# Optimization experiments

Hardware: AMD Instinct MI355X
Metric: run time of the kernel (lower is better)

The kernel has to match this reference:

```python
import jax, jax.numpy as jnp
from jax import lax
import numpy as np

B, C, O, NF, H, W = 4, 64, 64, 64, 128, 128
DK = 3
K = DK * DK
PAD = DK // 2


def setup_inputs() -> dict:
    key = jax.random.key(0)
    k0, k1, k2, k3 = jax.random.split(key, 4)
    inputs = jax.random.normal(k0, (B, C, H, W), jnp.float32)
    feat = jax.random.normal(k1, (B, NF, H, W), jnp.float32)
    # small offset-conv weights keep learned offsets in a realistic sub-pixel range
    om_w = jax.random.normal(k2, (C * 3 * K, NF, 3, 3), jnp.float32) * 0.02
    om_b = jnp.zeros((C * 3 * K,), jnp.float32)
    dc_w = jax.random.normal(k3, (O, C, DK, DK), jnp.float32) * (1.0 / np.sqrt(C * K))
    dc_b = jnp.zeros((O,), jnp.float32)
    return dict(inputs=inputs, feat=feat, om_w=om_w, om_b=om_b, dc_w=dc_w, dc_b=dc_b)


def _gather(img, y, x):
    # img: [B,C,H,W]; y,x: int32 [B,C,K,H,W]; zero outside bounds
    valid = (y >= 0) & (y < H) & (x >= 0) & (x < W)
    yc = jnp.clip(y, 0, H - 1)
    xc = jnp.clip(x, 0, W - 1)
    idx = (yc * W + xc).reshape(B, C, K, H * W)
    flat = img.reshape(B, C, 1, H * W)
    v = jnp.take_along_axis(flat, idx, axis=3).reshape(B, C, K, H, W)
    return jnp.where(valid, v, 0.0)


def _forward(inputs, feat, om_w, om_b, dc_w, dc_b):
    # offset/mask conv: nf -> in_nc*3*K, 3x3, pad 1
    off_msk = lax.conv_general_dilated(
        feat, om_w, (1, 1), ((1, 1), (1, 1)),
        dimension_numbers=('NCHW', 'OIHW', 'NCHW')) + om_b[None, :, None, None]
    # offsets interleaved (y,x) per kernel tap per deformable group (= channel)
    off = off_msk[:, :C * 2 * K].reshape(B, C, K, 2, H, W)
    msk = jax.nn.sigmoid(off_msk[:, C * 2 * K:]).reshape(B, C, K, H, W)

    ky = (jnp.arange(K) // DK - PAD).astype(jnp.float32)  # [K]
    kx = (jnp.arange(K) % DK - PAD).astype(jnp.float32)
    hg = jnp.arange(H, dtype=jnp.float32)
    wg = jnp.arange(W, dtype=jnp.float32)
    py = hg[None, None, None, :, None] + ky[None, None, :, None, None] + off[:, :, :, 0]  # [B,C,K,H,W]
    px = wg[None, None, None, None, :] + kx[None, None, :, None, None] + off[:, :, :, 1]

    y0f = jnp.floor(py); x0f = jnp.floor(px)
    wy = py - y0f; wx = px - x0f
    y0 = y0f.astype(jnp.int32); x0 = x0f.astype(jnp.int32)
    y1 = y0 + 1; x1 = x0 + 1

    v00 = _gather(inputs, y0, x0)
    v01 = _gather(inputs, y0, x1)
    v10 = _gather(inputs, y1, x0)
    v11 = _gather(inputs, y1, x1)
    sampled = ((1 - wy) * (1 - wx) * v00 + (1 - wy) * wx * v01
               + wy * (1 - wx) * v10 + wy * wx * v11) * msk  # [B,C,K,H,W]

    out = jnp.einsum('bckhw,ock->bohw', sampled, dc_w.reshape(O, C, K))
    out = out + dc_b[None, :, None, None]
    return jax.nn.relu(out)


def reference(inputs, feat, om_w, om_b, dc_w, dc_b):
    return _forward(inputs, feat, om_w, om_b, dc_w, dc_b)
```

## Files before the change

### kernel.cpp

```cpp
#include <hip/hip_runtime.h>
#include <hip/hip_bf16.h>

typedef __bf16 bf16;
typedef __bf16 bf16x8 __attribute__((ext_vector_type(8)));
typedef __bf16 bf16x4 __attribute__((ext_vector_type(4)));
typedef float f32x4 __attribute__((ext_vector_type(4)));
typedef float f32x2 __attribute__((ext_vector_type(2)));
typedef float f32x2u __attribute__((ext_vector_type(2))) __attribute__((aligned(4)));
typedef int  i32x4 __attribute__((ext_vector_type(4)));

#define MFMA16(a, b, c) __builtin_amdgcn_mfma_f32_16x16x32_bf16((a), (b), (c), 0, 0, 0)

static constexpr size_t FEATS_OFF = 0;
static constexpr size_t OMW3_OFF  = 8388608;
static constexpr size_t DCW_OFF   = OMW3_OFF + 1990656;
static constexpr size_t SC_OFF    = DCW_OFF + 73728;
static constexpr size_t PAD_OFF   = SC_OFF + 9216;


__global__ void prep_featS(const float* __restrict__ feat, bf16* __restrict__ featS) {
    const int hh = blockIdx.x, b = blockIdx.y;
    __shared__ float t[64][129];
    for (int i = threadIdx.x; i < 64 * 32; i += 256) {
        int cf = i >> 5, q = i & 31;
        const float* src = feat + ((size_t)(b * 64 + cf) * 128 + hh) * 128 + q * 4;
        t[cf][q * 4 + 0] = src[0];
        t[cf][q * 4 + 1] = src[1];
        t[cf][q * 4 + 2] = src[2];
        t[cf][q * 4 + 3] = src[3];
    }
    __syncthreads();
    for (int i = threadIdx.x; i < 1024; i += 256) {
        int px = i >> 3, cfb = i & 7;
        int sb = cfb ^ (px & 7);
        bf16x8 v;
#pragma unroll
        for (int e = 0; e < 8; ++e) v[e] = (bf16)t[cfb * 8 + e][px];
        *(bf16x8*)(featS + ((size_t)((b * 128 + hh) * 128 + px) << 6) + sb * 8) = v;
    }
}

__global__ void prep_weights(const float* __restrict__ om_w, const float* __restrict__ om_b,
                             const float* __restrict__ dc_w,
                             bf16* __restrict__ omw3, bf16* __restrict__ dcw2p,
                             float* __restrict__ scf) {
    int i = blockIdx.x * 256 + threadIdx.x;
    if (i < 995328) {
        int e = i & 511, lane = e >> 3, j = e & 7;
        int q = i >> 9;
        int t = q % 3, q2 = q / 3, kk = q2 % 18, ct = q2 / 18;
        int ck = ct * 16 + (lane & 15);
        int kcol = kk * 32 + (lane >> 4) * 8 + j;
        int tap = kcol >> 6, cf = kcol & 63;
        int ch = (t < 2) ? (ck * 2 + t) : (1152 + ck);
        omw3[i] = (bf16)om_w[ch * 576 + cf * 9 + tap];
    }
    if (i < 36864) {
        int j = i & 7, lane = (i >> 3) & 63, ot = (i >> 9) & 3, win = i >> 11;
        int o = ot * 16 + (lane & 15);
        int ck = win * 32 + (lane >> 4) * 8 + j;
        dcw2p[i] = (bf16)dc_w[o * 576 + ck];
    }
    if (i < 576) {
        int ck = i;
        int c = ck / 9, kd = ck - 9 * c, kq = kd / 3, kx = kd - 3 * kq;
        int pr = ck >> 1, lo = ck & 1;
        scf[pr * 8 + 0 + lo] = om_b[ck * 2]     + (float)(kq + 2);
        scf[pr * 8 + 2 + lo] = om_b[ck * 2 + 1] + (float)(kx + 2);
        scf[pr * 8 + 4 + lo] = om_b[1152 + ck];
        scf[pr * 8 + 6 + lo] = __uint_as_float((unsigned)(c * 17956));
    }
}

__global__ void prep_pad(const float* __restrict__ inputs, float* __restrict__ pad) {
    int yy = blockIdx.x, bc = blockIdx.y, xx = threadIdx.x;
    if (xx >= 134) return;
    float v = 0.f;
    if (yy >= 3 && yy <= 130 && xx >= 3 && xx <= 130)
        v = inputs[(size_t)bc * 16384 + (yy - 3) * 128 + (xx - 3)];
    pad[((size_t)bc * 134 + yy) * 134 + xx] = v;
}


__global__ void __launch_bounds__(256, 4)
deform_fused(const float* __restrict__ pad,
             const bf16* __restrict__ featS,
             const bf16* __restrict__ omw3,
             const bf16* __restrict__ dcw2p,
             const f32x4* __restrict__ sconst,
             const float* __restrict__ dcb,
             float* __restrict__ out)
{
    const int bid = blockIdx.x;
    const int P0 = (bid & 1) << 6;
    const int h = (bid >> 1) & 127;
    const int b = bid >> 8;
    const int tid = threadIdx.x;
    const int lane = tid & 63;
    const int wid_s = __builtin_amdgcn_readfirstlane(tid >> 6);
    const int l15 = lane & 15, g = lane >> 4;

    __shared__ __align__(16) unsigned char smem[25344 + 8192];
    char* featB = (char*)smem;
    char* sampB = (char*)smem + 25344;

    for (int i = tid; i < 6336; i += 256) ((unsigned*)featB)[i] = 0u;
    __syncthreads();
    {
        const int s0 = (P0 == 0) ? 0 : 63;
        const int q0 = (P0 == 0) ? 1 : 0;
        for (int i = tid; i < 1560; i += 256) {
            int ky = i / 520, rem = i - ky * 520, row = rem >> 3, c = rem & 7;
            int hh = h - 1 + ky;
            if ((unsigned)hh < 128u) {
                const char* src = (const char*)featS
                    + (((size_t)(b * 128 + hh) * 128 + s0 + row) << 7) + c * 16;
                *(i32x4*)(featB + ((ky * 66 + q0 + row) << 7) + c * 16) = *(const i32x4*)src;
            }
        }
    }
    __syncthreads();

    int fb[18];
#pragma unroll
    for (int kk = 0; kk < 18; ++kk) {
        const int tap = kk >> 1;
        const int kyp = tap / 3, kxp = tap - 3 * kyp;
        const int q = l15 + kxp;
        fb[kk] = (kyp * 66 + q) * 128 + ((((kk & 1) * 4 + g) ^ ((q + 7) & 7)) << 4);
    }

    f32x4 acc2[4];
#pragma unroll
    for (int u = 0; u < 4; ++u) acc2[u] = (f32x4){0.f, 0.f, 0.f, 0.f};

    const bf16* omw3_l = omw3 + lane * 8;
    const bf16* dcw_l  = dcw2p + lane * 8;
    const float* padb0 = pad + (size_t)b * 64 * 17956;
    const f32x2 hb2 = {(float)h, (float)h};
    const f32x2 fx2 = {(float)(P0 + l15), (float)(P0 + l15)};
    const int g4 = g * 4;

#pragma unroll 1
    for (int blk = 0; blk < 9; ++blk) {
        f32x4 acc1[3][4];
#pragma unroll
        for (int t = 0; t < 3; ++t)
#pragma unroll
            for (int nf = 0; nf < 4; ++nf) acc1[t][nf] = (f32x4){0.f, 0.f, 0.f, 0.f};

        const int abase = (blk * 4 + wid_s) * 27648;

#pragma unroll
        for (int kk = 0; kk < 18; ++kk) {
            bf16x8 a0 = *(const bf16x8*)(omw3_l + abase + ((kk * 3 + 0) << 9));
            bf16x8 a1 = *(const bf16x8*)(omw3_l + abase + ((kk * 3 + 1) << 9));
            bf16x8 a2 = *(const bf16x8*)(omw3_l + abase + ((kk * 3 + 2) << 9));
            bf16x8 bfr[4];
#pragma unroll
            for (int nf = 0; nf < 4; ++nf)
                bfr[nf] = *(const bf16x8*)(featB + fb[kk] + nf * 2048);
            __builtin_amdgcn_s_setprio(1);
#pragma unroll
            for (int nf = 0; nf < 4; ++nf) {
                acc1[0][nf] = MFMA16(a0, bfr[nf], acc1[0][nf]);
                acc1[1][nf] = MFMA16(a1, bfr[nf], acc1[1][nf]);
                acc1[2][nf] = MFMA16(a2, bfr[nf], acc1[2][nf]);
            }
            __builtin_amdgcn_s_setprio(0);
        }

        bf16x8 aK0 = *(const bf16x8*)(dcw_l + ((blk * 8 + wid_s) << 9));
        bf16x8 aK1 = *(const bf16x8*)(dcw_l + ((blk * 8 + 4 + wid_s) << 9));

        const f32x4* scB = sconst + (blk * 64 + wid_s * 16);
        f32x4 e0A = scB[g4 + 0], e1A = scB[g4 + 1];
        f32x4 e0B = scB[g4 + 2], e1B = scB[g4 + 3];
        f32x2 yb[2], xb[2], mb[2];
        unsigned co[2][2];
        yb[0] = f32x2{e0A.x, e0A.y} + hb2;
        xb[0] = f32x2{e0A.z, e0A.w} + fx2;
        mb[0] = f32x2{e1A.x, e1A.y};
        co[0][0] = __float_as_uint(e1A.z); co[0][1] = __float_as_uint(e1A.w);
        yb[1] = f32x2{e0B.x, e0B.y} + hb2;
        xb[1] = f32x2{e0B.z, e0B.w} + fx2;
        mb[1] = f32x2{e1B.x, e1B.y};
        co[1][0] = __float_as_uint(e1B.z); co[1][1] = __float_as_uint(e1B.w);

#pragma unroll
        for (int nf = 0; nf < 4; ++nf) {
            float s[4];
#pragma unroll
            for (int pi = 0; pi < 2; ++pi) {
                f32x2 py = f32x2{acc1[0][nf][2 * pi], acc1[0][nf][2 * pi + 1]} + yb[pi];
                f32x2 px = f32x2{acc1[1][nf][2 * pi], acc1[1][nf][2 * pi + 1]} + xb[pi];
                f32x2 lg = f32x2{acc1[2][nf][2 * pi], acc1[2][nf][2 * pi + 1]} + mb[pi];
#pragma unroll
                for (int e = 0; e < 2; ++e) {
                    float pyc = __builtin_amdgcn_fmed3f(py[e], 0.5f, 132.5f);
                    float pxc = __builtin_amdgcn_fmed3f(px[e], 0.5f, 132.5f);
                    int y0 = (int)pyc, x0 = (int)pxc;
                    float wy = __builtin_amdgcn_fractf(pyc);
                    float wx = __builtin_amdgcn_fractf(pxc);
                    unsigned off = co[pi][e] + (unsigned)(y0 * 134 + x0);
                    f32x2u t0 = *(const f32x2u*)(padb0 + off);
                    f32x2u t1 = *(const f32x2u*)(padb0 + off + 134);
                    float top = t0.x + wx * (t0.y - t0.x);
                    float bot = t1.x + wx * (t1.y - t1.x);
                    float bil = top + wy * (bot - top);
                    float mk = __builtin_amdgcn_rcpf(1.f + __expf(-lg[e]));
                    s[2 * pi + e] = bil * mk;
                }
            }
            bf16x4 pk4 = {(bf16)s[0], (bf16)s[1], (bf16)s[2], (bf16)s[3]};
            *(bf16x4*)(sampB + (nf * 16 + l15) * 128
                       + (((wid_s * 4 + g) ^ ((l15 & 7) << 1)) << 3)) = pk4;
            xb[0] += 16.f; xb[1] += 16.f;
        }
        __syncthreads();

        const int rb_swz = (g ^ (l15 & 7)) << 4;
        __builtin_amdgcn_s_setprio(1);
#pragma unroll
        for (int u = 0; u < 4; ++u) {
            const int rb = (u * 16 + l15) * 128 + rb_swz;
            bf16x8 b0 = *(const bf16x8*)(sampB + rb);
            bf16x8 b1 = *(const bf16x8*)(sampB + (rb ^ 64));
            acc2[u] = MFMA16(aK0, b0, acc2[u]);
            acc2[u] = MFMA16(aK1, b1, acc2[u]);
        }
        __builtin_amdgcn_s_setprio(0);
        __syncthreads();
    }

    float bias[4];
#pragma unroll
    for (int r = 0; r < 4; ++r) bias[r] = dcb[wid_s * 16 + g * 4 + r];
#pragma unroll
    for (int u = 0; u < 4; ++u)
#pragma unroll
        for (int r = 0; r < 4; ++r) {
            int o = wid_s * 16 + g * 4 + r;
            out[((size_t)(b * 64 + o) * 128 + h) * 128 + P0 + u * 16 + l15]
                = fmaxf(acc2[u][r] + bias[r], 0.f);
        }
}

extern "C" void kernel_launch(void* const* d_in, const int* in_sizes, int n_in,
                              void* d_out, int out_size, void* d_ws, size_t ws_size,
                              hipStream_t stream) {
    const float* inputs = (const float*)d_in[0];
    const float* feat   = (const float*)d_in[1];
    const float* om_w   = (const float*)d_in[2];
    const float* om_b   = (const float*)d_in[3];
    const float* dc_w   = (const float*)d_in[4];
    const float* dc_b   = (const float*)d_in[5];
    float* out = (float*)d_out;

    char* ws = (char*)d_ws;
    bf16*  featS  = (bf16*)(ws + FEATS_OFF);
    bf16*  omw3   = (bf16*)(ws + OMW3_OFF);
    bf16*  dcw2p  = (bf16*)(ws + DCW_OFF);
    float* scf    = (float*)(ws + SC_OFF);
    float* pad    = (float*)(ws + PAD_OFF);

    prep_featS<<<dim3(128, 4), 256, 0, stream>>>(feat, featS);
    prep_weights<<<(995328 + 255) / 256, 256, 0, stream>>>(om_w, om_b, dc_w, omw3, dcw2p, scf);
    prep_pad<<<dim3(134, 256), 256, 0, stream>>>(inputs, pad);

    deform_fused<<<1024, 256, 0, stream>>>(pad, featS, omw3, dcw2p,
                                           (const f32x4*)scf, dc_b, out);
}
```

Before: 177.2 us.

## Feed sampled values to the second GEMM straight from registers, reducing across waves

Result: slower. 248.1 us (+40.0%).

```diff
diff --git a/kernel.cpp b/kernel.cpp
--- a/kernel.cpp
+++ b/kernel.cpp
@@ -13,8 +13,8 @@
 
 static constexpr size_t FEATS_OFF = 0;
 static constexpr size_t OMW3_OFF  = 8388608;
-static constexpr size_t DCW_OFF   = OMW3_OFF + 1990656;
-static constexpr size_t SC_OFF    = DCW_OFF + 73728;
+static constexpr size_t DCWT_OFF  = OMW3_OFF + 1990656;
+static constexpr size_t SC_OFF    = DCWT_OFF + 81920;
 static constexpr size_t PAD_OFF   = SC_OFF + 9216;
 
 
@@ -42,7 +42,7 @@
 
 __global__ void prep_weights(const float* __restrict__ om_w, const float* __restrict__ om_b,
                              const float* __restrict__ dc_w,
-                             bf16* __restrict__ omw3, bf16* __restrict__ dcw2p,
+                             bf16* __restrict__ omw3, bf16* __restrict__ dcwt,
                              float* __restrict__ scf) {
     int i = blockIdx.x * 256 + threadIdx.x;
     if (i < 995328) {
@@ -55,11 +55,18 @@
         int ch = (t < 2) ? (ck * 2 + t) : (1152 + ck);
         omw3[i] = (bf16)om_w[ch * 576 + cf * 9 + tap];
     }
-    if (i < 36864) {
-        int j = i & 7, lane = (i >> 3) & 63, ot = (i >> 9) & 3, win = i >> 11;
-        int o = ot * 16 + (lane & 15);
-        int ck = win * 32 + (lane >> 4) * 8 + j;
-        dcw2p[i] = (bf16)dc_w[o * 576 + ck];
+    if (i < 40960) {
+        int j = i & 7, lane = (i >> 3) & 63, ot = (i >> 9) & 3, wid = (i >> 11) & 3, pair = i >> 13;
+        int o = ot * 16 + (lane & 15), gq = lane >> 4;
+        float v = 0.f;
+        if (pair < 4) {
+            int ck = pair * 128 + wid * 16 + gq * 4 + ((j < 4) ? j : j + 60);
+            v = dc_w[o * 576 + ck];
+        } else if (j < 4) {
+            int ck = 512 + wid * 16 + gq * 4 + j;
+            v = dc_w[o * 576 + ck];
+        }
+        dcwt[i] = (bf16)v;
     }
     if (i < 576) {
         int ck = i;
@@ -82,11 +89,11 @@
 }
 
 
-__global__ void __launch_bounds__(256, 4)
+__global__ void __launch_bounds__(256, 3)
 deform_fused(const float* __restrict__ pad,
              const bf16* __restrict__ featS,
              const bf16* __restrict__ omw3,
-             const bf16* __restrict__ dcw2p,
+             const bf16* __restrict__ dcwt,
              const f32x4* __restrict__ sconst,
              const float* __restrict__ dcb,
              float* __restrict__ out)
@@ -100,9 +107,8 @@
     const int wid_s = __builtin_amdgcn_readfirstlane(tid >> 6);
     const int l15 = lane & 15, g = lane >> 4;
 
-    __shared__ __align__(16) unsigned char smem[25344 + 8192];
+    __shared__ __align__(16) unsigned char smem[33792];
     char* featB = (char*)smem;
-    char* sampB = (char*)smem + 25344;
 
     for (int i = tid; i < 6336; i += 256) ((unsigned*)featB)[i] = 0u;
     __syncthreads();
@@ -121,28 +127,28 @@
     }
     __syncthreads();
 
-    int fb[18];
-#pragma unroll
-    for (int kk = 0; kk < 18; ++kk) {
-        const int tap = kk >> 1;
+    int fb9[9];
+#pragma unroll
+    for (int tap = 0; tap < 9; ++tap) {
         const int kyp = tap / 3, kxp = tap - 3 * kyp;
         const int q = l15 + kxp;
-        fb[kk] = (kyp * 66 + q) * 128 + ((((kk & 1) * 4 + g) ^ ((q + 7) & 7)) << 4);
-    }
-
-    f32x4 acc2[4];
-#pragma unroll
-    for (int u = 0; u < 4; ++u) acc2[u] = (f32x4){0.f, 0.f, 0.f, 0.f};
+        fb9[tap] = (kyp * 66 + q) * 128 + ((g ^ ((q + 7) & 7)) << 4);
+    }
+
+    f32x4 acc2[4][4];
+#pragma unroll
+    for (int ot = 0; ot < 4; ++ot)
+#pragma unroll
+        for (int nf = 0; nf < 4; ++nf) acc2[ot][nf] = (f32x4){0.f, 0.f, 0.f, 0.f};
 
     const bf16* omw3_l = omw3 + lane * 8;
-    const bf16* dcw_l  = dcw2p + lane * 8;
+    const bf16* dcwt_l = dcwt + lane * 8;
     const float* padb0 = pad + (size_t)b * 64 * 17956;
     const f32x2 hb2 = {(float)h, (float)h};
     const f32x2 fx2 = {(float)(P0 + l15), (float)(P0 + l15)};
     const int g4 = g * 4;
 
-#pragma unroll 1
-    for (int blk = 0; blk < 9; ++blk) {
+    auto do_block = [&](int blk, bf16x4* pdst) {
         f32x4 acc1[3][4];
 #pragma unroll
         for (int t = 0; t < 3; ++t)
@@ -156,10 +162,11 @@
             bf16x8 a0 = *(const bf16x8*)(omw3_l + abase + ((kk * 3 + 0) << 9));
             bf16x8 a1 = *(const bf16x8*)(omw3_l + abase + ((kk * 3 + 1) << 9));
             bf16x8 a2 = *(const bf16x8*)(omw3_l + abase + ((kk * 3 + 2) << 9));
+            const int base = fb9[kk >> 1] ^ ((kk & 1) << 6);
             bf16x8 bfr[4];
 #pragma unroll
             for (int nf = 0; nf < 4; ++nf)
-                bfr[nf] = *(const bf16x8*)(featB + fb[kk] + nf * 2048);
+                bfr[nf] = *(const bf16x8*)(featB + base + nf * 2048);
             __builtin_amdgcn_s_setprio(1);
 #pragma unroll
             for (int nf = 0; nf < 4; ++nf) {
@@ -169,9 +176,6 @@
             }
             __builtin_amdgcn_s_setprio(0);
         }
-
-        bf16x8 aK0 = *(const bf16x8*)(dcw_l + ((blk * 8 + wid_s) << 9));
-        bf16x8 aK1 = *(const bf16x8*)(dcw_l + ((blk * 8 + 4 + wid_s) << 9));
 
         const f32x4* scB = sconst + (blk * 64 + wid_s * 16);
         f32x4 e0A = scB[g4 + 0], e1A = scB[g4 + 1];
@@ -212,38 +216,85 @@
                     s[2 * pi + e] = bil * mk;
                 }
             }
-            bf16x4 pk4 = {(bf16)s[0], (bf16)s[1], (bf16)s[2], (bf16)s[3]};
-            *(bf16x4*)(sampB + (nf * 16 + l15) * 128
-                       + (((wid_s * 4 + g) ^ ((l15 & 7) << 1)) << 3)) = pk4;
+            pdst[nf] = (bf16x4){(bf16)s[0], (bf16)s[1], (bf16)s[2], (bf16)s[3]};
             xb[0] += 16.f; xb[1] += 16.f;
         }
-        __syncthreads();
-
-        const int rb_swz = (g ^ (l15 & 7)) << 4;
+    };
+
+    bf16x4 pE[4], pO[4];
+
+#pragma unroll 1
+    for (int pair = 0; pair < 4; ++pair) {
+        do_block(2 * pair, pE);
+        do_block(2 * pair + 1, pO);
+        const bf16* aKb = dcwt_l + (((pair * 4 + wid_s) * 4) << 9);
+        bf16x8 aK0 = *(const bf16x8*)(aKb);
+        bf16x8 aK1 = *(const bf16x8*)(aKb + 512);
+        bf16x8 aK2 = *(const bf16x8*)(aKb + 1024);
+        bf16x8 aK3 = *(const bf16x8*)(aKb + 1536);
         __builtin_amdgcn_s_setprio(1);
 #pragma unroll
-        for (int u = 0; u < 4; ++u) {
-            const int rb = (u * 16 + l15) * 128 + rb_swz;
-            bf16x8 b0 = *(const bf16x8*)(sampB + rb);
-            bf16x8 b1 = *(const bf16x8*)(sampB + (rb ^ 64));
-            acc2[u] = MFMA16(aK0, b0, acc2[u]);
-            acc2[u] = MFMA16(aK1, b1, acc2[u]);
+        for (int nf = 0; nf < 4; ++nf) {
+            bf16x8 bfr = __builtin_shufflevector(pE[nf], pO[nf], 0, 1, 2, 3, 4, 5, 6, 7);
+            acc2[0][nf] = MFMA16(aK0, bfr, acc2[0][nf]);
+            acc2[1][nf] = MFMA16(aK1, bfr, acc2[1][nf]);
+            acc2[2][nf] = MFMA16(aK2, bfr, acc2[2][nf]);
+            acc2[3][nf] = MFMA16(aK3, bfr, acc2[3][nf]);
         }
         __builtin_amdgcn_s_setprio(0);
-        __syncthreads();
-    }
-
-    float bias[4];
-#pragma unroll
-    for (int r = 0; r < 4; ++r) bias[r] = dcb[wid_s * 16 + g * 4 + r];
-#pragma unroll
-    for (int u = 0; u < 4; ++u)
-#pragma unroll
-        for (int r = 0; r < 4; ++r) {
-            int o = wid_s * 16 + g * 4 + r;
-            out[((size_t)(b * 64 + o) * 128 + h) * 128 + P0 + u * 16 + l15]
-                = fmaxf(acc2[u][r] + bias[r], 0.f);
-        }
+    }
+    do_block(8, pE);
+    {
+        const bf16 z = (bf16)0.f;
+        bf16x4 zz = {z, z, z, z};
+#pragma unroll
+        for (int nf = 0; nf < 4; ++nf) pO[nf] = zz;
+    }
+    {
+        const bf16* aKb = dcwt_l + (((4 * 4 + wid_s) * 4) << 9);
+        bf16x8 aK0 = *(const bf16x8*)(aKb);
+        bf16x8 aK1 = *(const bf16x8*)(aKb + 512);
+        bf16x8 aK2 = *(const bf16x8*)(aKb + 1024);
+        bf16x8 aK3 = *(const bf16x8*)(aKb + 1536);
+#pragma unroll
+        for (int nf = 0; nf < 4; ++nf) {
+            bf16x8 bfr = __builtin_shufflevector(pE[nf], pO[nf], 0, 1, 2, 3, 4, 5, 6, 7);
+            acc2[0][nf] = MFMA16(aK0, bfr, acc2[0][nf]);
+            acc2[1][nf] = MFMA16(aK1, bfr, acc2[1][nf]);
+            acc2[2][nf] = MFMA16(aK2, bfr, acc2[2][nf]);
+            acc2[3][nf] = MFMA16(aK3, bfr, acc2[3][nf]);
+        }
+    }
+
+    __syncthreads();
+    float* red0 = (float*)smem;
+    float* red1 = (float*)smem + 4224;
+    float* mybuf = (wid_s & 1) ? red1 : red0;
+    if (wid_s < 2) {
+#pragma unroll
+        for (int ot = 0; ot < 4; ++ot)
+#pragma unroll
+            for (int nf = 0; nf < 4; ++nf)
+#pragma unroll
+                for (int r = 0; r < 4; ++r)
+                    mybuf[(ot * 16 + g * 4 + r) * 66 + nf * 16 + l15] = acc2[ot][nf][r];
+    }
+    __syncthreads();
+    if (wid_s >= 2) {
+#pragma unroll
+        for (int ot = 0; ot < 4; ++ot)
+#pragma unroll
+            for (int nf = 0; nf < 4; ++nf)
+#pragma unroll
+                for (int r = 0; r < 4; ++r)
+                    mybuf[(ot * 16 + g * 4 + r) * 66 + nf * 16 + l15] += acc2[ot][nf][r];
+    }
+    __syncthreads();
+    for (int it = tid; it < 4096; it += 256) {
+        int o = it >> 6, px = it & 63;
+        float v = red0[o * 66 + px] + red1[o * 66 + px] + dcb[o];
+        out[((size_t)(b * 64 + o) * 128 + h) * 128 + P0 + px] = fmaxf(v, 0.f);
+    }
 }
 
 extern "C" void kernel_launch(void* const* d_in, const int* in_sizes, int n_in,
@@ -260,14 +311,14 @@
     char* ws = (char*)d_ws;
     bf16*  featS  = (bf16*)(ws + FEATS_OFF);
     bf16*  omw3   = (bf16*)(ws + OMW3_OFF);
-    bf16*  dcw2p  = (bf16*)(ws + DCW_OFF);
+    bf16*  dcwt   = (bf16*)(ws + DCWT_OFF);
     float* scf    = (float*)(ws + SC_OFF);
     float* pad    = (float*)(ws + PAD_OFF);
 
     prep_featS<<<dim3(128, 4), 256, 0, stream>>>(feat, featS);
-    prep_weights<<<(995328 + 255) / 256, 256, 0, stream>>>(om_w, om_b, dc_w, omw3, dcw2p, scf);
+    prep_weights<<<(995328 + 255) / 256, 256, 0, stream>>>(om_w, om_b, dc_w, omw3, dcwt, scf);
     prep_pad<<<dim3(134, 256), 256, 0, stream>>>(inputs, pad);
 
-    deform_fused<<<1024, 256, 0, stream>>>(pad, featS, omw3, dcw2p,
+    deform_fused<<<1024, 256, 0, stream>>>(pad, featS, omw3, dcwt,
                                            (const f32x4*)scf, dc_b, out);
 }
```

## Split sampling into two halves and defer second-half MFMA to overlap next block

Applied to the files above, without the earlier changes.

Result: slower. 185.6 us (+4.8%).

```diff
diff --git a/kernel.cpp b/kernel.cpp
--- a/kernel.cpp
+++ b/kernel.cpp
@@ -100,9 +100,10 @@
     const int wid_s = __builtin_amdgcn_readfirstlane(tid >> 6);
     const int l15 = lane & 15, g = lane >> 4;
 
-    __shared__ __align__(16) unsigned char smem[25344 + 8192];
+    __shared__ __align__(16) unsigned char smem[33792];
     char* featB = (char*)smem;
-    char* sampB = (char*)smem + 25344;
+    char* buf0  = (char*)smem + 25344;
+    char* buf1  = (char*)smem + 29440;
 
     for (int i = tid; i < 6336; i += 256) ((unsigned*)featB)[i] = 0u;
     __syncthreads();
@@ -121,13 +122,12 @@
     }
     __syncthreads();
 
-    int fb[18];
-#pragma unroll
-    for (int kk = 0; kk < 18; ++kk) {
-        const int tap = kk >> 1;
+    int fb9[9];
+#pragma unroll
+    for (int tap = 0; tap < 9; ++tap) {
         const int kyp = tap / 3, kxp = tap - 3 * kyp;
         const int q = l15 + kxp;
-        fb[kk] = (kyp * 66 + q) * 128 + ((((kk & 1) * 4 + g) ^ ((q + 7) & 7)) << 4);
+        fb9[tap] = (kyp * 66 + q) * 128 + ((g ^ ((q + 7) & 7)) << 4);
     }
 
     f32x4 acc2[4];
@@ -140,9 +140,26 @@
     const f32x2 hb2 = {(float)h, (float)h};
     const f32x2 fx2 = {(float)(P0 + l15), (float)(P0 + l15)};
     const int g4 = g * 4;
+    const int rswz = (g ^ (l15 & 7)) << 4;
+    const int wswz = ((wid_s * 4 + g) ^ ((l15 & 7) << 1)) << 3;
+
+    bf16x8 aKp0, aKp1;
 
 #pragma unroll 1
     for (int blk = 0; blk < 9; ++blk) {
+        if (blk > 0) {
+            __builtin_amdgcn_s_setprio(1);
+#pragma unroll
+            for (int u = 2; u < 4; ++u) {
+                const int rb = ((u - 2) * 16 + l15) * 128 + rswz;
+                bf16x8 b0 = *(const bf16x8*)(buf1 + rb);
+                bf16x8 b1 = *(const bf16x8*)(buf1 + (rb ^ 64));
+                acc2[u] = MFMA16(aKp0, b0, acc2[u]);
+                acc2[u] = MFMA16(aKp1, b1, acc2[u]);
+            }
+            __builtin_amdgcn_s_setprio(0);
+        }
+
         f32x4 acc1[3][4];
 #pragma unroll
         for (int t = 0; t < 3; ++t)
@@ -150,16 +167,16 @@
             for (int nf = 0; nf < 4; ++nf) acc1[t][nf] = (f32x4){0.f, 0.f, 0.f, 0.f};
 
         const int abase = (blk * 4 + wid_s) * 27648;
-
 #pragma unroll
         for (int kk = 0; kk < 18; ++kk) {
             bf16x8 a0 = *(const bf16x8*)(omw3_l + abase + ((kk * 3 + 0) << 9));
             bf16x8 a1 = *(const bf16x8*)(omw3_l + abase + ((kk * 3 + 1) << 9));
             bf16x8 a2 = *(const bf16x8*)(omw3_l + abase + ((kk * 3 + 2) << 9));
+            const int base = fb9[kk >> 1] ^ ((kk & 1) << 6);
             bf16x8 bfr[4];
 #pragma unroll
             for (int nf = 0; nf < 4; ++nf)
-                bfr[nf] = *(const bf16x8*)(featB + fb[kk] + nf * 2048);
+                bfr[nf] = *(const bf16x8*)(featB + base + nf * 2048);
             __builtin_amdgcn_s_setprio(1);
 #pragma unroll
             for (int nf = 0; nf < 4; ++nf) {
@@ -187,13 +204,13 @@
         mb[1] = f32x2{e1B.x, e1B.y};
         co[1][0] = __float_as_uint(e1B.z); co[1][1] = __float_as_uint(e1B.w);
 
-#pragma unroll
-        for (int nf = 0; nf < 4; ++nf) {
+        auto sample_nf = [&](int nf, char* dst) {
+            const f32x2 nfo = {16.f * (float)nf, 16.f * (float)nf};
             float s[4];
 #pragma unroll
             for (int pi = 0; pi < 2; ++pi) {
                 f32x2 py = f32x2{acc1[0][nf][2 * pi], acc1[0][nf][2 * pi + 1]} + yb[pi];
-                f32x2 px = f32x2{acc1[1][nf][2 * pi], acc1[1][nf][2 * pi + 1]} + xb[pi];
+                f32x2 px = f32x2{acc1[1][nf][2 * pi], acc1[1][nf][2 * pi + 1]} + xb[pi] + nfo;
                 f32x2 lg = f32x2{acc1[2][nf][2 * pi], acc1[2][nf][2 * pi + 1]} + mb[pi];
 #pragma unroll
                 for (int e = 0; e < 2; ++e) {
@@ -213,24 +230,37 @@
                 }
             }
             bf16x4 pk4 = {(bf16)s[0], (bf16)s[1], (bf16)s[2], (bf16)s[3]};
-            *(bf16x4*)(sampB + (nf * 16 + l15) * 128
-                       + (((wid_s * 4 + g) ^ ((l15 & 7) << 1)) << 3)) = pk4;
-            xb[0] += 16.f; xb[1] += 16.f;
-        }
+            *(bf16x4*)(dst + ((nf & 1) * 16 + l15) * 128 + wswz) = pk4;
+        };
+
+        sample_nf(0, buf0);
+        sample_nf(1, buf0);
         __syncthreads();
 
-        const int rb_swz = (g ^ (l15 & 7)) << 4;
         __builtin_amdgcn_s_setprio(1);
 #pragma unroll
-        for (int u = 0; u < 4; ++u) {
-            const int rb = (u * 16 + l15) * 128 + rb_swz;
-            bf16x8 b0 = *(const bf16x8*)(sampB + rb);
-            bf16x8 b1 = *(const bf16x8*)(sampB + (rb ^ 64));
+        for (int u = 0; u < 2; ++u) {
+            const int rb = (u * 16 + l15) * 128 + rswz;
+            bf16x8 b0 = *(const bf16x8*)(buf0 + rb);
+            bf16x8 b1 = *(const bf16x8*)(buf0 + (rb ^ 64));
             acc2[u] = MFMA16(aK0, b0, acc2[u]);
             acc2[u] = MFMA16(aK1, b1, acc2[u]);
         }
         __builtin_amdgcn_s_setprio(0);
+        sample_nf(2, buf1);
+        sample_nf(3, buf1);
         __syncthreads();
+
+        aKp0 = aK0; aKp1 = aK1;
+    }
+
+#pragma unroll
+    for (int u = 2; u < 4; ++u) {
+        const int rb = ((u - 2) * 16 + l15) * 128 + rswz;
+        bf16x8 b0 = *(const bf16x8*)(buf1 + rb);
+        bf16x8 b1 = *(const bf16x8*)(buf1 + (rb ^ 64));
+        acc2[u] = MFMA16(aKp0, b0, acc2[u]);
+        acc2[u] = MFMA16(aKp1, b1, acc2[u]);
     }
 
     float bias[4];
```

## Double-buffer sampled tile and defer second GEMM to drop a barrier per block

Applied to the files above, without the earlier changes.

Result: slower. 204.8 us (+15.6%).

```diff
diff --git a/kernel.cpp b/kernel.cpp
--- a/kernel.cpp
+++ b/kernel.cpp
@@ -82,7 +82,7 @@
 }
 
 
-__global__ void __launch_bounds__(256, 4)
+__global__ void __launch_bounds__(256, 3)
 deform_fused(const float* __restrict__ pad,
              const bf16* __restrict__ featS,
              const bf16* __restrict__ omw3,
@@ -100,9 +100,10 @@
     const int wid_s = __builtin_amdgcn_readfirstlane(tid >> 6);
     const int l15 = lane & 15, g = lane >> 4;
 
-    __shared__ __align__(16) unsigned char smem[25344 + 8192];
+    __shared__ __align__(16) unsigned char smem[41728];
     char* featB = (char*)smem;
-    char* sampB = (char*)smem + 25344;
+    char* bufA  = (char*)smem + 25344;
+    char* bufB  = (char*)smem + 33536;
 
     for (int i = tid; i < 6336; i += 256) ((unsigned*)featB)[i] = 0u;
     __syncthreads();
@@ -121,13 +122,12 @@
     }
     __syncthreads();
 
-    int fb[18];
-#pragma unroll
-    for (int kk = 0; kk < 18; ++kk) {
-        const int tap = kk >> 1;
+    int fb9[9];
+#pragma unroll
+    for (int tap = 0; tap < 9; ++tap) {
         const int kyp = tap / 3, kxp = tap - 3 * kyp;
         const int q = l15 + kxp;
-        fb[kk] = (kyp * 66 + q) * 128 + ((((kk & 1) * 4 + g) ^ ((q + 7) & 7)) << 4);
+        fb9[tap] = (kyp * 66 + q) * 128 + ((g ^ ((q + 7) & 7)) << 4);
     }
 
     f32x4 acc2[4];
@@ -140,9 +140,29 @@
     const f32x2 hb2 = {(float)h, (float)h};
     const f32x2 fx2 = {(float)(P0 + l15), (float)(P0 + l15)};
     const int g4 = g * 4;
+    const int rswz = (g ^ (l15 & 7)) << 4;
+    const int wswz = ((wid_s * 4 + g) ^ ((l15 & 7) << 1)) << 3;
 
 #pragma unroll 1
     for (int blk = 0; blk < 9; ++blk) {
+        char* bcur  = (blk & 1) ? bufB : bufA;
+        char* bprev = (blk & 1) ? bufA : bufB;
+
+        if (blk > 0) {
+            bf16x8 aK0 = *(const bf16x8*)(dcw_l + (((blk - 1) * 8 + wid_s) << 9));
+            bf16x8 aK1 = *(const bf16x8*)(dcw_l + (((blk - 1) * 8 + 4 + wid_s) << 9));
+            __builtin_amdgcn_s_setprio(1);
+#pragma unroll
+            for (int u = 0; u < 4; ++u) {
+                const int rb = (u * 16 + l15) * 128 + rswz;
+                bf16x8 b0 = *(const bf16x8*)(bprev + rb);
+                bf16x8 b1 = *(const bf16x8*)(bprev + (rb ^ 64));
+                acc2[u] = MFMA16(aK0, b0, acc2[u]);
+                acc2[u] = MFMA16(aK1, b1, acc2[u]);
+            }
+            __builtin_amdgcn_s_setprio(0);
+        }
+
         f32x4 acc1[3][4];
 #pragma unroll
         for (int t = 0; t < 3; ++t)
@@ -150,16 +170,16 @@
             for (int nf = 0; nf < 4; ++nf) acc1[t][nf] = (f32x4){0.f, 0.f, 0.f, 0.f};
 
         const int abase = (blk * 4 + wid_s) * 27648;
-
 #pragma unroll
         for (int kk = 0; kk < 18; ++kk) {
             bf16x8 a0 = *(const bf16x8*)(omw3_l + abase + ((kk * 3 + 0) << 9));
             bf16x8 a1 = *(const bf16x8*)(omw3_l + abase + ((kk * 3 + 1) << 9));
             bf16x8 a2 = *(const bf16x8*)(omw3_l + abase + ((kk * 3 + 2) << 9));
+            const int base = fb9[kk >> 1] ^ ((kk & 1) << 6);
             bf16x8 bfr[4];
 #pragma unroll
             for (int nf = 0; nf < 4; ++nf)
-                bfr[nf] = *(const bf16x8*)(featB + fb[kk] + nf * 2048);
+                bfr[nf] = *(const bf16x8*)(featB + base + nf * 2048);
             __builtin_amdgcn_s_setprio(1);
 #pragma unroll
             for (int nf = 0; nf < 4; ++nf) {
@@ -169,9 +189,6 @@
             }
             __builtin_amdgcn_s_setprio(0);
         }
-
-        bf16x8 aK0 = *(const bf16x8*)(dcw_l + ((blk * 8 + wid_s) << 9));
-        bf16x8 aK1 = *(const bf16x8*)(dcw_l + ((blk * 8 + 4 + wid_s) << 9));
 
         const f32x4* scB = sconst + (blk * 64 + wid_s * 16);
         f32x4 e0A = scB[g4 + 0], e1A = scB[g4 + 1];
@@ -213,24 +230,23 @@
                 }
             }
             bf16x4 pk4 = {(bf16)s[0], (bf16)s[1], (bf16)s[2], (bf16)s[3]};
-            *(bf16x4*)(sampB + (nf * 16 + l15) * 128
-                       + (((wid_s * 4 + g) ^ ((l15 & 7) << 1)) << 3)) = pk4;
+            *(bf16x4*)(bcur + (nf * 16 + l15) * 128 + wswz) = pk4;
             xb[0] += 16.f; xb[1] += 16.f;
         }
         __syncthreads();
-
-        const int rb_swz = (g ^ (l15 & 7)) << 4;
-        __builtin_amdgcn_s_setprio(1);
+    }
+
+    {
+        bf16x8 aK0 = *(const bf16x8*)(dcw_l + ((8 * 8 + wid_s) << 9));
+        bf16x8 aK1 = *(const bf16x8*)(dcw_l + ((8 * 8 + 4 + wid_s) << 9));
 #pragma unroll
         for (int u = 0; u < 4; ++u) {
-            const int rb = (u * 16 + l15) * 128 + rb_swz;
-            bf16x8 b0 = *(const bf16x8*)(sampB + rb);
-            bf16x8 b1 = *(const bf16x8*)(sampB + (rb ^ 64));
+            const int rb = (u * 16 + l15) * 128 + rswz;
+            bf16x8 b0 = *(const bf16x8*)(bufA + rb);
+            bf16x8 b1 = *(const bf16x8*)(bufA + (rb ^ 64));
             acc2[u] = MFMA16(aK0, b0, acc2[u]);
             acc2[u] = MFMA16(aK1, b1, acc2[u]);
         }
-        __builtin_amdgcn_s_setprio(0);
-        __syncthreads();
     }
 
     float bias[4];
```
